# Optimization experiments

Hardware: AMD Instinct MI355X
Metric: run time of the kernel (lower is better)

Reference implementation:

```python
import jax, jax.numpy as jnp
import numpy as np

VOCAB = 8192
BETA = 0.25


def setup_inputs() -> dict:
    key = jax.random.key(0)
    k1, k2 = jax.random.split(key)
    x = jax.random.normal(k1, (16, 1024, 256), dtype=jnp.float32)
    emb = jax.random.normal(k2, (256, VOCAB), dtype=jnp.float32) * 0.05  # xavier-ish scale
    return {"x": x, "emb": emb}


def reference(x, emb):
    C = x.shape[-1]
    x_flat = x.reshape(-1, C)  # [M, C]
    M = x_flat.shape[0]
    distances = ((x_flat ** 2).sum(axis=1, keepdims=True)
                 - 2.0 * jnp.einsum('mc,ck->mk', x_flat, emb)
                 + (emb ** 2).sum(axis=0, keepdims=True))
    # argmax(-d) == argmin(d), same first-occurrence tie-break
    encoding_indices = jnp.argmin(distances, axis=-1)  # [M]
    # direct gather instead of one-hot @ emb (same math)
    quantized = jnp.take(emb, encoding_indices, axis=1).T  # [M, C]
    quantized = quantized.reshape(x.shape)
    e_latent_loss = ((jax.lax.stop_gradient(quantized) - x) ** 2).mean()
    q_latent_loss = ((quantized - jax.lax.stop_gradient(x)) ** 2).mean()
    loss_vq = q_latent_loss + BETA * e_latent_loss
    quantized = x + jax.lax.stop_gradient(quantized - x)  # straight-through
    # avg_probs == one_hot(indices).mean(0) -> normalized histogram
    counts = jnp.zeros((VOCAB,), dtype=x.dtype).at[encoding_indices].add(1.0)
    avg_probs = counts / M
    perplexity = jnp.exp(-jnp.sum(avg_probs * jnp.log(avg_probs + 1e-10)))
    return quantized, loss_vq, perplexity
```

## Files before the change

### kernel.cpp

```cpp
#include <hip/hip_runtime.h>
#include <cfloat>
#include <cmath>

#define VOCAB 8192
#define MTOT 16384
#define CDIM 256
#define BM 64
#define KSPLIT 8
#define KRANGE (VOCAB / KSPLIT)
#define TAU 0.1f
#define IDX_INF 0x7fffffff

typedef __attribute__((ext_vector_type(8))) short bf16x8;
typedef __attribute__((ext_vector_type(4))) float f32x4;

#define AS1 __attribute__((address_space(1)))
#define AS3 __attribute__((address_space(3)))

__device__ __forceinline__ void gl_lds16(const void* g, void* l) {
  __builtin_amdgcn_global_load_lds((const AS1 unsigned int*)g,
                                   (AS3 unsigned int*)l, 16, 0, 0);
}

__device__ inline ushort f2bf(float f) {
  unsigned u = __float_as_uint(f);
  unsigned r = (u + 0x7fffu + ((u >> 16) & 1u)) >> 16;
  return (ushort)r;
}

__device__ __forceinline__ void ins4(uint& k0, uint& k1, uint& k2, uint& k3, uint a) {
  uint t;
  t = min(k0, a); a = max(k0, a); k0 = t;
  t = min(k1, a); a = max(k1, a); k1 = t;
  t = min(k2, a); a = max(k2, a); k2 = t;
  k3 = min(k3, a);
}

__global__ void vq_enorm_kernel(const float* __restrict__ emb,
                                float* __restrict__ enorm16,
                                double* __restrict__ enormd) {
  __shared__ double sd[4][64];
  int tid = threadIdx.x;
  int kk = tid & 63, cg = tid >> 6;
  int k = blockIdx.x * 64 + kk;
  double s = 0.0;
  for (int c = cg * 64; c < cg * 64 + 64; ++c) {
    float v = emb[(size_t)c * VOCAB + k];
    s += (double)v * (double)v;
  }
  sd[cg][kk] = s;
  __syncthreads();
  if (cg == 0) {
    double t = sd[0][kk] + sd[1][kk] + sd[2][kk] + sd[3][kk];
    enorm16[k] = (float)t + 16.0f;
    enormd[k] = t;
  }
}

__global__ void vq_prep_embT_kernel(const float* __restrict__ emb,
                                    float* __restrict__ embT) {
  __shared__ float t[32][33];
  int bc = blockIdx.x & 7;
  int bk = blockIdx.x >> 3;
  int lx = threadIdx.x & 31, lyq = threadIdx.x >> 5;
#pragma unroll
  for (int yy = 0; yy < 4; ++yy) {
    int y = lyq * 4 + yy;
    t[y][lx] = emb[(size_t)(bc * 32 + y) * VOCAB + bk * 32 + lx];
  }
  __syncthreads();
#pragma unroll
  for (int yy = 0; yy < 4; ++yy) {
    int y = lyq * 4 + yy;
    embT[(size_t)(bk * 32 + y) * CDIM + bc * 32 + lx] = t[lx][y];
  }
}

__global__ void vq_pack_x_kernel(const float* __restrict__ x,
                                 ushort* __restrict__ xb) {
  int u = blockIdx.x * 256 + threadIdx.x;
  int rb = u >> 11;
  int q = u & 2047;
  int cc = q >> 9, row = (q >> 3) & 63, sw = q & 7;
  int c0 = cc * 64 + ((sw ^ (row & 7)) << 3);
  const float* src = x + (size_t)(rb * 64 + row) * CDIM + c0;
  float4 v0 = *(const float4*)src;
  float4 v1 = *(const float4*)(src + 4);
  float a[8] = {v0.x, v0.y, v0.z, v0.w, v1.x, v1.y, v1.z, v1.w};
  bf16x8 h;
#pragma unroll
  for (int j = 0; j < 8; ++j) h[j] = (short)f2bf(-2.0f * a[j]);
  *(bf16x8*)(xb + (size_t)u * 8) = h;
}

__global__ void vq_pack_e_kernel(const float* __restrict__ embT,
                                 ushort* __restrict__ eb) {
  int u = blockIdx.x * 256 + threadIdx.x;
  int kbcc = u >> 10;
  int q = u & 1023;
  int code = q >> 3, sw = q & 7;
  int kb2 = kbcc >> 2, cc = kbcc & 3;
  int c0 = cc * 64 + ((sw ^ (code & 7)) << 3);
  const float* src = embT + (size_t)(kb2 * 128 + code) * CDIM + c0;
  float4 v0 = *(const float4*)src;
  float4 v1 = *(const float4*)(src + 4);
  float a[8] = {v0.x, v0.y, v0.z, v0.w, v1.x, v1.y, v1.z, v1.w};
  bf16x8 h;
#pragma unroll
  for (int j = 0; j < 8; ++j) h[j] = (short)f2bf(a[j]);
  *(bf16x8*)(eb + (size_t)u * 8) = h;
}

__global__ __launch_bounds__(256, 2) void vq_dist_bf16_kernel(
    const ushort* __restrict__ xb, const ushort* __restrict__ eb,
    const float* __restrict__ en16g, uint4* __restrict__ pk) {
  __shared__ ushort Asw[4 * 64 * 64];
  __shared__ ushort Bsw[2 * 128 * 64];

  const int tid = threadIdx.x;
  const int lane = tid & 63, wid = tid >> 6;
  const int wr = wid >> 1, wc = wid & 1;
  const int l15 = lane & 15, lg = lane >> 4;
  const int rb = blockIdx.x >> 3, sp = blockIdx.x & 7;
  const int m0 = rb * BM;

  uint baA[2][2], baB[4][2];
#pragma unroll
  for (int mf = 0; mf < 2; ++mf) {
    int row = wr * 32 + mf * 16 + l15;
#pragma unroll
    for (int kh = 0; kh < 2; ++kh)
      baA[mf][kh] = row * 128 + ((((kh * 4) + lg) ^ (row & 7)) << 4);
  }
#pragma unroll
  for (int nf = 0; nf < 4; ++nf) {
    int code = wc * 64 + nf * 16 + l15;
#pragma unroll
    for (int kh = 0; kh < 2; ++kh)
      baB[nf][kh] = code * 128 + ((((kh * 4) + lg) ^ (code & 7)) << 4);
  }

  const uint plB = wid * 2048 + lane * 8;
  const ushort* ebk = eb + (size_t)sp * 262144;

  {
    const ushort* xs = xb + (size_t)rb * 16384;
#pragma unroll
    for (int i = 0; i < 8; ++i) {
      int seg = wid * 8 + i;
      gl_lds16(xs + (size_t)seg * 512 + lane * 8, &Asw[seg * 512]);
    }
#pragma unroll
    for (int i = 0; i < 4; ++i)
      gl_lds16(ebk + plB + i * 512, &Bsw[(wid * 4 + i) * 512]);
  }

  const int nb = sp * KRANGE + wc * 64 + l15;
  uint kmin[8];
#pragma unroll
  for (int s = 0; s < 8; ++s) kmin[s] = 0xffffffffu;

  f32x4 acc[2][4];

  for (int kt = 0; kt < 8; ++kt) {
    float e16[4];
#pragma unroll
    for (int nf = 0; nf < 4; ++nf) e16[nf] = en16g[nb + kt * 128 + nf * 16];
#pragma unroll
    for (int mf = 0; mf < 2; ++mf)
#pragma unroll
      for (int nf = 0; nf < 4; ++nf)
        acc[mf][nf] = (f32x4){e16[nf], e16[nf], e16[nf], e16[nf]};

#pragma unroll
    for (int cc = 0; cc < 4; ++cc) {
      __syncthreads();
      if (cc < 3 || kt < 7) {
        const ushort* src = ebk + (cc + 1) * 8192 + plB;
        ushort* dst = &Bsw[((cc + 1) & 1) * 8192 + (wid * 4) * 512];
#pragma unroll
        for (int i = 0; i < 4; ++i)
          gl_lds16(src + i * 512, dst + i * 512);
      }
      const char* Ab = (const char*)Asw + cc * 8192;
      const char* Bb = (const char*)Bsw + (cc & 1) * 16384;
#pragma unroll
      for (int kh = 0; kh < 2; ++kh) {
        bf16x8 af[2], bfr[4];
#pragma unroll
        for (int mf = 0; mf < 2; ++mf)
          af[mf] = *(const bf16x8*)(Ab + baA[mf][kh]);
#pragma unroll
        for (int nf = 0; nf < 4; ++nf)
          bfr[nf] = *(const bf16x8*)(Bb + baB[nf][kh]);
#pragma unroll
        for (int mf = 0; mf < 2; ++mf)
#pragma unroll
          for (int nf = 0; nf < 4; ++nf)
            acc[mf][nf] = __builtin_amdgcn_mfma_f32_16x16x32_bf16(af[mf], bfr[nf], acc[mf][nf], 0, 0, 0);
      }
    }
#pragma unroll
    for (int nf = 0; nf < 4; ++nf) {
      uint nk = (uint)(nb + kt * 128 + nf * 16);
#pragma unroll
      for (int mf = 0; mf < 2; ++mf)
#pragma unroll
        for (int r = 0; r < 4; ++r) {
          uint u = __float_as_uint(acc[mf][nf][r]) & 0xffffe000u;
          kmin[mf * 4 + r] = min(kmin[mf * 4 + r], u | nk);
        }
    }
    ebk += 32768;
  }

  __syncthreads();
  uint* karr = (uint*)Asw;
#pragma unroll
  for (int mf = 0; mf < 2; ++mf)
#pragma unroll
    for (int r = 0; r < 4; ++r) {
      int row = wr * 32 + mf * 16 + lg * 4 + r;
      karr[(wc * 64 + row) * 17 + l15] = kmin[mf * 4 + r];
    }
  __syncthreads();
  if (tid < BM) {
    uint k0 = ~0u, k1 = ~0u, k2 = ~0u, k3 = ~0u;
    const uint* r0 = karr + tid * 17;
    const uint* r1 = karr + (64 + tid) * 17;
#pragma unroll
    for (int j = 0; j < 16; ++j) ins4(k0, k1, k2, k3, r0[j]);
#pragma unroll
    for (int j = 0; j < 16; ++j) ins4(k0, k1, k2, k3, r1[j]);
    pk[(size_t)sp * MTOT + m0 + tid] = make_uint4(k0, k1, k2, k3);
  }
}

__global__ void vq_gather_kernel(
    const float* __restrict__ x, const float* __restrict__ embT,
    const double* __restrict__ enormd, const uint4* __restrict__ pk,
    float* __restrict__ out, int* __restrict__ counts, float* __restrict__ ssep) {
  const int wid = threadIdx.x >> 6, lane = threadIdx.x & 63;
  const int m = blockIdx.x * 4 + wid;

  const float4 xq = *(const float4*)(x + (size_t)m * CDIM + lane * 4);

  float bd = FLT_MAX, sd = FLT_MAX;
  uint bkey = 0xffffffffu;
#pragma unroll
  for (int sp2 = 0; sp2 < KSPLIT; ++sp2) {
    uint4 kv = pk[(size_t)sp2 * MTOT + m];
    uint ks[4] = {kv.x, kv.y, kv.z, kv.w};
#pragma unroll
    for (int j = 0; j < 4; ++j) {
      uint k = ks[j];
      float dq = __uint_as_float(k & 0xffffe000u);
      if (k < bkey) { sd = bd; bd = dq; bkey = k; }
      else sd = fminf(sd, dq);
    }
  }
  int best = (int)(bkey & 8191u);
  if (sd - bd < TAU) {
    double bD = DBL_MAX;
    int bn = IDX_INF;
    for (int sp2 = 0; sp2 < KSPLIT; ++sp2) {
      uint4 kv = pk[(size_t)sp2 * MTOT + m];
      uint ks[4] = {kv.x, kv.y, kv.z, kv.w};
#pragma unroll
      for (int j = 0; j < 4; ++j) {
        int cj = (int)(ks[j] & 8191u);
        const float4 ev = *(const float4*)(embT + (size_t)cj * CDIM + lane * 4);
        double p = (double)xq.x * ev.x + (double)xq.y * ev.y
                 + (double)xq.z * ev.z + (double)xq.w * ev.w;
#pragma unroll
        for (int off = 1; off < 64; off <<= 1) p += __shfl_xor(p, off, 64);
        double dj = enormd[cj] - 2.0 * p;
        if (dj < bD || (dj == bD && cj < bn)) { bD = dj; bn = cj; }
      }
    }
    best = bn;
  }
  const float4 ev = *(const float4*)(embT + (size_t)best * CDIM + lane * 4);
  *(float4*)(out + (size_t)m * CDIM + lane * 4) = ev;
  float dx = ev.x - xq.x, dy = ev.y - xq.y, dz = ev.z - xq.z, dw = ev.w - xq.w;
  float v = dx * dx + dy * dy + dz * dz + dw * dw;
#pragma unroll
  for (int off = 32; off > 0; off >>= 1) v += __shfl_down(v, off, 64);
  if (lane == 0) {
    ssep[m] = v;
    atomicAdd(&counts[best], 1);
  }
}

__global__ void vq_final1_kernel(const float* __restrict__ ssep,
                                 const int* __restrict__ counts,
                                 double* __restrict__ part) {
  __shared__ double red[256];
  const int tid = threadIdx.x, b = blockIdx.x;
  red[tid] = (double)ssep[b * 256 + tid];
  __syncthreads();
  for (int off = 128; off > 0; off >>= 1) {
    if (tid < off) red[tid] += red[tid + off];
    __syncthreads();
  }
  if (tid == 0) part[b] = red[0];
  __syncthreads();
  double e = 0.0;
  if (tid < 128) {
    double p = (double)counts[b * 128 + tid] / (double)MTOT;
    e = p * log(p + 1e-10);
  }
  red[tid] = e;
  __syncthreads();
  for (int off = 128; off > 0; off >>= 1) {
    if (tid < off) red[tid] += red[tid + off];
    __syncthreads();
  }
  if (tid == 0) part[64 + b] = red[0];
}

__global__ void vq_final2_kernel(const double* __restrict__ part,
                                 float* __restrict__ out) {
  const int lane = threadIdx.x;
  double s = part[lane], e = part[64 + lane];
#pragma unroll
  for (int off = 32; off > 0; off >>= 1) {
    s += __shfl_down(s, off, 64);
    e += __shfl_down(e, off, 64);
  }
  if (lane == 0) {
    out[(size_t)MTOT * CDIM] = (float)(1.25 * s / (double)((size_t)MTOT * CDIM));
    out[(size_t)MTOT * CDIM + 1] = (float)exp(-e);
  }
}

extern "C" void kernel_launch(void* const* d_in, const int* in_sizes, int n_in,
                              void* d_out, int out_size, void* d_ws, size_t ws_size,
                              hipStream_t stream) {
  const float* x = (const float*)d_in[0];
  const float* emb = (const float*)d_in[1];
  float* out = (float*)d_out;
  char* ws = (char*)d_ws;

  double* enormd = (double*)(ws);
  float* enorm16 = (float*)(ws + 65536);
  uint4* pk      = (uint4*)(ws + 98304);
  int* counts    = (int*)(ws + 2195456);
  float* ssep    = (float*)(ws + 2228224);
  double* part   = (double*)(ws + 2293760);
  float* embT    = (float*)(ws + 2294784);
  ushort* xb     = (ushort*)(ws + 10683392);
  ushort* eb     = (ushort*)(ws + 19072000);

  hipMemsetAsync(counts, 0, VOCAB * sizeof(int), stream);
  vq_enorm_kernel<<<VOCAB / 64, 256, 0, stream>>>(emb, enorm16, enormd);
  vq_prep_embT_kernel<<<(VOCAB / 32) * (CDIM / 32), 256, 0, stream>>>(emb, embT);
  vq_pack_e_kernel<<<(VOCAB * CDIM / 8) / 256, 256, 0, stream>>>(embT, eb);
  vq_pack_x_kernel<<<(MTOT * CDIM / 8) / 256, 256, 0, stream>>>(x, xb);
  vq_dist_bf16_kernel<<<(MTOT / BM) * KSPLIT, 256, 0, stream>>>(xb, eb, enorm16, pk);
  vq_gather_kernel<<<MTOT / 4, 256, 0, stream>>>(x, embT, enormd, pk, out, counts, ssep);
  vq_final1_kernel<<<64, 256, 0, stream>>>(ssep, counts, part);
  vq_final2_kernel<<<1, 64, 0, stream>>>(part, out);
}
```

Measured before the change: 169.3 us.

## Enlarge distance GEMM tile to 128 rows with 8 waves and split key storage

Restructures the bf16 distance kernel from 64-row tiles and 4 waves to 128-row tiles with 512 threads, each wave computing a 64x128 sub-tile. The x and embedding packing are reorganised into a new pair-interleaved swizzled layout, so each B chunk is reused across more rows and fewer blocks reload the codebook. The packed float/index keys (masked distance plus +16 offset) are replaced by separate float distance and int index arrays with explicit tie-breaking, and the top-4 candidates are reduced in two stages. This raises register pressure (acc[4][8] plus 16 best slots) and LDS use, and doubles the candidate buffer traffic to the gather kernel.

```diff
diff --git a/kernel.cpp b/kernel.cpp
--- a/kernel.cpp
+++ b/kernel.cpp
@@ -5,9 +5,7 @@
 #define VOCAB 8192
 #define MTOT 16384
 #define CDIM 256
-#define BM 64
 #define KSPLIT 8
-#define KRANGE (VOCAB / KSPLIT)
 #define TAU 0.1f
 #define IDX_INF 0x7fffffff
 
@@ -28,16 +26,8 @@
   return (ushort)r;
 }
 
-__device__ __forceinline__ void ins4(uint& k0, uint& k1, uint& k2, uint& k3, uint a) {
-  uint t;
-  t = min(k0, a); a = max(k0, a); k0 = t;
-  t = min(k1, a); a = max(k1, a); k1 = t;
-  t = min(k2, a); a = max(k2, a); k2 = t;
-  k3 = min(k3, a);
-}
-
 __global__ void vq_enorm_kernel(const float* __restrict__ emb,
-                                float* __restrict__ enorm16,
+                                float* __restrict__ enorm,
                                 double* __restrict__ enormd) {
   __shared__ double sd[4][64];
   int tid = threadIdx.x;
@@ -52,7 +42,7 @@
   __syncthreads();
   if (cg == 0) {
     double t = sd[0][kk] + sd[1][kk] + sd[2][kk] + sd[3][kk];
-    enorm16[k] = (float)t + 16.0f;
+    enorm[k] = (float)t;
     enormd[k] = t;
   }
 }
@@ -79,11 +69,14 @@
 __global__ void vq_pack_x_kernel(const float* __restrict__ x,
                                  ushort* __restrict__ xb) {
   int u = blockIdx.x * 256 + threadIdx.x;
-  int rb = u >> 11;
-  int q = u & 2047;
-  int cc = q >> 9, row = (q >> 3) & 63, sw = q & 7;
-  int c0 = cc * 64 + ((sw ^ (row & 7)) << 3);
-  const float* src = x + (size_t)(rb * 64 + row) * CDIM + c0;
+  int rb = u >> 12;
+  int o = u & 4095;
+  int cc = o >> 9, w = o & 511;
+  int pair = w >> 3, sswz = w & 7;
+  int s = sswz ^ (pair & 7);
+  int row = pair * 2 + (s >> 2);
+  int g = s & 3;
+  const float* src = x + (size_t)(rb * 128 + row) * CDIM + cc * 32 + g * 8;
   float4 v0 = *(const float4*)src;
   float4 v1 = *(const float4*)(src + 4);
   float a[8] = {v0.x, v0.y, v0.z, v0.w, v1.x, v1.y, v1.z, v1.w};
@@ -96,12 +89,18 @@
 __global__ void vq_pack_e_kernel(const float* __restrict__ embT,
                                  ushort* __restrict__ eb) {
   int u = blockIdx.x * 256 + threadIdx.x;
-  int kbcc = u >> 10;
-  int q = u & 1023;
-  int code = q >> 3, sw = q & 7;
-  int kb2 = kbcc >> 2, cc = kbcc & 3;
-  int c0 = cc * 64 + ((sw ^ (code & 7)) << 3);
-  const float* src = embT + (size_t)(kb2 * 128 + code) * CDIM + c0;
+  int sp = u >> 15;
+  int r = u & 32767;
+  int ct = (r >> 14) & 1, chunk = (r >> 11) & 7;
+  int o16 = r & 2047;
+  int wcg = o16 >> 9, w = o16 & 511;
+  int pair = w >> 3, sswz = w & 7;
+  int s = sswz ^ (pair & 7);
+  int cloc = pair * 2 + (s >> 2);
+  int g = s & 3;
+  int code = sp * 1024 + ct * 512 + wcg * 128 + cloc;
+  int dims = chunk * 32 + g * 8;
+  const float* src = embT + (size_t)code * CDIM + dims;
   float4 v0 = *(const float4*)src;
   float4 v1 = *(const float4*)(src + 4);
   float a[8] = {v0.x, v0.y, v0.z, v0.w, v1.x, v1.y, v1.z, v1.w};
@@ -111,134 +110,163 @@
   *(bf16x8*)(eb + (size_t)u * 8) = h;
 }
 
-__global__ __launch_bounds__(256, 2) void vq_dist_bf16_kernel(
+__global__ __launch_bounds__(512, 2) void vq_dist_kernel(
     const ushort* __restrict__ xb, const ushort* __restrict__ eb,
-    const float* __restrict__ en16g, uint4* __restrict__ pk) {
-  __shared__ ushort Asw[4 * 64 * 64];
-  __shared__ ushort Bsw[2 * 128 * 64];
+    const float* __restrict__ enorm,
+    float4* __restrict__ pkd, int4* __restrict__ pki) {
+  __shared__ ushort Abuf[32768];
+  __shared__ ushort Bbuf[2][16384];
 
   const int tid = threadIdx.x;
   const int lane = tid & 63, wid = tid >> 6;
-  const int wr = wid >> 1, wc = wid & 1;
+  const int wr = wid >> 2, wc = wid & 3;
   const int l15 = lane & 15, lg = lane >> 4;
   const int rb = blockIdx.x >> 3, sp = blockIdx.x & 7;
-  const int m0 = rb * BM;
-
-  uint baA[2][2], baB[4][2];
-#pragma unroll
-  for (int mf = 0; mf < 2; ++mf) {
-    int row = wr * 32 + mf * 16 + l15;
-#pragma unroll
-    for (int kh = 0; kh < 2; ++kh)
-      baA[mf][kh] = row * 128 + ((((kh * 4) + lg) ^ (row & 7)) << 4);
-  }
-#pragma unroll
-  for (int nf = 0; nf < 4; ++nf) {
-    int code = wc * 64 + nf * 16 + l15;
-#pragma unroll
-    for (int kh = 0; kh < 2; ++kh)
-      baB[nf][kh] = code * 128 + ((((kh * 4) + lg) ^ (code & 7)) << 4);
-  }
-
-  const uint plB = wid * 2048 + lane * 8;
-  const ushort* ebk = eb + (size_t)sp * 262144;
+  const int m0 = rb * 128;
+  const int spbase = sp * 1024;
 
   {
-    const ushort* xs = xb + (size_t)rb * 16384;
-#pragma unroll
-    for (int i = 0; i < 8; ++i) {
-      int seg = wid * 8 + i;
-      gl_lds16(xs + (size_t)seg * 512 + lane * 8, &Asw[seg * 512]);
-    }
+    const ushort* xs = xb + (size_t)rb * 32768;
+#pragma unroll
+    for (int i = 0; i < 8; ++i)
+      gl_lds16(xs + (wid * 8 + i) * 512 + lane * 8, &Abuf[(wid * 8 + i) * 512]);
+    const ushort* bs = eb + (size_t)sp * 262144;
 #pragma unroll
     for (int i = 0; i < 4; ++i)
-      gl_lds16(ebk + plB + i * 512, &Bsw[(wid * 4 + i) * 512]);
-  }
-
-  const int nb = sp * KRANGE + wc * 64 + l15;
-  uint kmin[8];
-#pragma unroll
-  for (int s = 0; s < 8; ++s) kmin[s] = 0xffffffffu;
-
-  f32x4 acc[2][4];
-
-  for (int kt = 0; kt < 8; ++kt) {
-    float e16[4];
-#pragma unroll
-    for (int nf = 0; nf < 4; ++nf) e16[nf] = en16g[nb + kt * 128 + nf * 16];
-#pragma unroll
-    for (int mf = 0; mf < 2; ++mf)
-#pragma unroll
-      for (int nf = 0; nf < 4; ++nf)
+      gl_lds16(bs + (wid * 4 + i) * 512 + lane * 8, &Bbuf[0][(wid * 4 + i) * 512]);
+  }
+
+  uint offA[4], offB[8];
+#pragma unroll
+  for (int mf = 0; mf < 4; ++mf) {
+    int row = wr * 64 + mf * 16 + l15;
+    int pr = row >> 1, s = ((row & 1) << 2) | lg;
+    offA[mf] = pr * 128 + ((s ^ (pr & 7)) << 4);
+  }
+#pragma unroll
+  for (int nf = 0; nf < 8; ++nf) {
+    int cl = nf * 16 + l15;
+    int pr = cl >> 1, s = ((cl & 1) << 2) | lg;
+    offB[nf] = wc * 8192 + pr * 128 + ((s ^ (pr & 7)) << 4);
+  }
+
+  float bv[16];
+  int bi[16];
+#pragma unroll
+  for (int s = 0; s < 16; ++s) { bv[s] = FLT_MAX; bi[s] = IDX_INF; }
+
+#pragma unroll
+  for (int ct = 0; ct < 2; ++ct) {
+    float e16[8];
+#pragma unroll
+    for (int nf = 0; nf < 8; ++nf)
+      e16[nf] = enorm[spbase + ct * 512 + wc * 128 + nf * 16 + l15];
+    f32x4 acc[4][8];
+#pragma unroll
+    for (int mf = 0; mf < 4; ++mf)
+#pragma unroll
+      for (int nf = 0; nf < 8; ++nf)
         acc[mf][nf] = (f32x4){e16[nf], e16[nf], e16[nf], e16[nf]};
 
 #pragma unroll
-    for (int cc = 0; cc < 4; ++cc) {
+    for (int cc = 0; cc < 8; ++cc) {
+      const int step = ct * 8 + cc;
       __syncthreads();
-      if (cc < 3 || kt < 7) {
-        const ushort* src = ebk + (cc + 1) * 8192 + plB;
-        ushort* dst = &Bsw[((cc + 1) & 1) * 8192 + (wid * 4) * 512];
+      if (step < 15) {
+        const ushort* bs = eb + (size_t)sp * 262144 + (size_t)(step + 1) * 16384;
+        ushort* dst = &Bbuf[(step + 1) & 1][0];
 #pragma unroll
         for (int i = 0; i < 4; ++i)
-          gl_lds16(src + i * 512, dst + i * 512);
+          gl_lds16(bs + (wid * 4 + i) * 512 + lane * 8, dst + (wid * 4 + i) * 512);
       }
-      const char* Ab = (const char*)Asw + cc * 8192;
-      const char* Bb = (const char*)Bsw + (cc & 1) * 16384;
-#pragma unroll
-      for (int kh = 0; kh < 2; ++kh) {
-        bf16x8 af[2], bfr[4];
-#pragma unroll
-        for (int mf = 0; mf < 2; ++mf)
-          af[mf] = *(const bf16x8*)(Ab + baA[mf][kh]);
-#pragma unroll
-        for (int nf = 0; nf < 4; ++nf)
-          bfr[nf] = *(const bf16x8*)(Bb + baB[nf][kh]);
-#pragma unroll
-        for (int mf = 0; mf < 2; ++mf)
-#pragma unroll
-          for (int nf = 0; nf < 4; ++nf)
-            acc[mf][nf] = __builtin_amdgcn_mfma_f32_16x16x32_bf16(af[mf], bfr[nf], acc[mf][nf], 0, 0, 0);
+      const char* Ab = (const char*)Abuf + cc * 8192;
+      const char* Bb = (const char*)&Bbuf[cc & 1][0];
+      bf16x8 af[4];
+#pragma unroll
+      for (int mf = 0; mf < 4; ++mf) af[mf] = *(const bf16x8*)(Ab + offA[mf]);
+#pragma unroll
+      for (int nf = 0; nf < 8; ++nf) {
+        bf16x8 bfr = *(const bf16x8*)(Bb + offB[nf]);
+#pragma unroll
+        for (int mf = 0; mf < 4; ++mf)
+          acc[mf][nf] = __builtin_amdgcn_mfma_f32_16x16x32_bf16(af[mf], bfr, acc[mf][nf], 0, 0, 0);
       }
     }
 #pragma unroll
-    for (int nf = 0; nf < 4; ++nf) {
-      uint nk = (uint)(nb + kt * 128 + nf * 16);
-#pragma unroll
-      for (int mf = 0; mf < 2; ++mf)
+    for (int nf = 0; nf < 8; ++nf) {
+      int n = spbase + ct * 512 + wc * 128 + nf * 16 + l15;
+#pragma unroll
+      for (int mf = 0; mf < 4; ++mf)
 #pragma unroll
         for (int r = 0; r < 4; ++r) {
-          uint u = __float_as_uint(acc[mf][nf][r]) & 0xffffe000u;
-          kmin[mf * 4 + r] = min(kmin[mf * 4 + r], u | nk);
+          float d = acc[mf][nf][r];
+          int s = mf * 4 + r;
+          if (d < bv[s]) { bv[s] = d; bi[s] = n; }
         }
     }
-    ebk += 32768;
-  }
-
-  __syncthreads();
-  uint* karr = (uint*)Asw;
-#pragma unroll
-  for (int mf = 0; mf < 2; ++mf)
+  }
+
+  __syncthreads();
+  float* kd = (float*)Abuf;
+  int* ki = (int*)Abuf + 8192;
+#pragma unroll
+  for (int mf = 0; mf < 4; ++mf)
 #pragma unroll
     for (int r = 0; r < 4; ++r) {
-      int row = wr * 32 + mf * 16 + lg * 4 + r;
-      karr[(wc * 64 + row) * 17 + l15] = kmin[mf * 4 + r];
-    }
-  __syncthreads();
-  if (tid < BM) {
-    uint k0 = ~0u, k1 = ~0u, k2 = ~0u, k3 = ~0u;
-    const uint* r0 = karr + tid * 17;
-    const uint* r1 = karr + (64 + tid) * 17;
-#pragma unroll
-    for (int j = 0; j < 16; ++j) ins4(k0, k1, k2, k3, r0[j]);
-#pragma unroll
-    for (int j = 0; j < 16; ++j) ins4(k0, k1, k2, k3, r1[j]);
-    pk[(size_t)sp * MTOT + m0 + tid] = make_uint4(k0, k1, k2, k3);
+      int row = wr * 64 + mf * 16 + lg * 4 + r;
+      int idx = (wc * 128 + row) * 16 + l15;
+      kd[idx] = bv[mf * 4 + r];
+      ki[idx] = bi[mf * 4 + r];
+    }
+  __syncthreads();
+  float* kod = (float*)&Bbuf[0][0];
+  int* koi = (int*)&Bbuf[0][0] + 1024;
+  {
+    int row = tid >> 2, part = tid & 3;
+    const float* rd = kd + (part * 128 + row) * 16;
+    const int* ri = ki + (part * 128 + row) * 16;
+    float d0 = FLT_MAX, d1 = FLT_MAX;
+    int i0 = IDX_INF, i1 = IDX_INF;
+#pragma unroll
+    for (int j = 0; j < 16; ++j) {
+      float a = rd[j];
+      int ai = ri[j];
+      if (a < d0 || (a == d0 && ai < i0)) { d1 = d0; i1 = i0; d0 = a; i0 = ai; }
+      else if (a < d1 || (a == d1 && ai < i1)) { d1 = a; i1 = ai; }
+    }
+    int o = (row * 4 + part) * 2;
+    kod[o] = d0; kod[o + 1] = d1;
+    koi[o] = i0; koi[o + 1] = i1;
+  }
+  __syncthreads();
+  if (tid < 128) {
+    const float* rd = kod + tid * 8;
+    const int* ri = koi + tid * 8;
+    float d[4] = {FLT_MAX, FLT_MAX, FLT_MAX, FLT_MAX};
+    int ix[4] = {IDX_INF, IDX_INF, IDX_INF, IDX_INF};
+#pragma unroll
+    for (int j = 0; j < 8; ++j) {
+      float a = rd[j];
+      int ai = ri[j];
+#pragma unroll
+      for (int q = 0; q < 4; ++q) {
+        bool lt = (a < d[q]) || (a == d[q] && ai < ix[q]);
+        float td = lt ? d[q] : a;
+        int ti = lt ? ix[q] : ai;
+        d[q] = lt ? a : d[q];
+        ix[q] = lt ? ai : ix[q];
+        a = td; ai = ti;
+      }
+    }
+    pkd[(size_t)sp * MTOT + m0 + tid] = make_float4(d[0], d[1], d[2], d[3]);
+    pki[(size_t)sp * MTOT + m0 + tid] = make_int4(ix[0], ix[1], ix[2], ix[3]);
   }
 }
 
 __global__ void vq_gather_kernel(
     const float* __restrict__ x, const float* __restrict__ embT,
-    const double* __restrict__ enormd, const uint4* __restrict__ pk,
+    const double* __restrict__ enormd,
+    const float4* __restrict__ pkd, const int4* __restrict__ pki,
     float* __restrict__ out, int* __restrict__ counts, float* __restrict__ ssep) {
   const int wid = threadIdx.x >> 6, lane = threadIdx.x & 63;
   const int m = blockIdx.x * 4 + wid;
@@ -246,29 +274,31 @@
   const float4 xq = *(const float4*)(x + (size_t)m * CDIM + lane * 4);
 
   float bd = FLT_MAX, sd = FLT_MAX;
-  uint bkey = 0xffffffffu;
+  int bidx = IDX_INF;
 #pragma unroll
   for (int sp2 = 0; sp2 < KSPLIT; ++sp2) {
-    uint4 kv = pk[(size_t)sp2 * MTOT + m];
-    uint ks[4] = {kv.x, kv.y, kv.z, kv.w};
+    float4 dv = pkd[(size_t)sp2 * MTOT + m];
+    int4 iv = pki[(size_t)sp2 * MTOT + m];
+    float ds[4] = {dv.x, dv.y, dv.z, dv.w};
+    int is[4] = {iv.x, iv.y, iv.z, iv.w};
 #pragma unroll
     for (int j = 0; j < 4; ++j) {
-      uint k = ks[j];
-      float dq = __uint_as_float(k & 0xffffe000u);
-      if (k < bkey) { sd = bd; bd = dq; bkey = k; }
-      else sd = fminf(sd, dq);
-    }
-  }
-  int best = (int)(bkey & 8191u);
+      float dj = ds[j];
+      int ij = is[j];
+      if (dj < bd || (dj == bd && ij < bidx)) { sd = bd; bd = dj; bidx = ij; }
+      else sd = fminf(sd, dj);
+    }
+  }
+  int best = bidx;
   if (sd - bd < TAU) {
     double bD = DBL_MAX;
     int bn = IDX_INF;
     for (int sp2 = 0; sp2 < KSPLIT; ++sp2) {
-      uint4 kv = pk[(size_t)sp2 * MTOT + m];
-      uint ks[4] = {kv.x, kv.y, kv.z, kv.w};
+      int4 iv = pki[(size_t)sp2 * MTOT + m];
+      int is[4] = {iv.x, iv.y, iv.z, iv.w};
 #pragma unroll
       for (int j = 0; j < 4; ++j) {
-        int cj = (int)(ks[j] & 8191u);
+        int cj = is[j];
         const float4 ev = *(const float4*)(embT + (size_t)cj * CDIM + lane * 4);
         double p = (double)xq.x * ev.x + (double)xq.y * ev.y
                  + (double)xq.z * ev.z + (double)xq.w * ev.w;
@@ -343,22 +373,24 @@
   char* ws = (char*)d_ws;
 
   double* enormd = (double*)(ws);
-  float* enorm16 = (float*)(ws + 65536);
-  uint4* pk      = (uint4*)(ws + 98304);
-  int* counts    = (int*)(ws + 2195456);
-  float* ssep    = (float*)(ws + 2228224);
-  double* part   = (double*)(ws + 2293760);
-  float* embT    = (float*)(ws + 2294784);
-  ushort* xb     = (ushort*)(ws + 10683392);
-  ushort* eb     = (ushort*)(ws + 19072000);
+  float* enorm   = (float*)(ws + 65536);
+  float4* pkd    = (float4*)(ws + 98304);
+  int4* pki      = (int4*)(ws + 2195456);
+  int* counts    = (int*)(ws + 4292608);
+  float* ssep    = (float*)(ws + 4325376);
+  double* part   = (double*)(ws + 4390912);
+  float* embT    = (float*)(ws + 4391936);
+  ushort* xb     = (ushort*)(ws + 12780544);
+  ushort* eb     = (ushort*)(ws + 21169152);
 
   hipMemsetAsync(counts, 0, VOCAB * sizeof(int), stream);
-  vq_enorm_kernel<<<VOCAB / 64, 256, 0, stream>>>(emb, enorm16, enormd);
+  vq_enorm_kernel<<<VOCAB / 64, 256, 0, stream>>>(emb, enorm, enormd);
   vq_prep_embT_kernel<<<(VOCAB / 32) * (CDIM / 32), 256, 0, stream>>>(emb, embT);
   vq_pack_e_kernel<<<(VOCAB * CDIM / 8) / 256, 256, 0, stream>>>(embT, eb);
   vq_pack_x_kernel<<<(MTOT * CDIM / 8) / 256, 256, 0, stream>>>(x, xb);
-  vq_dist_bf16_kernel<<<(MTOT / BM) * KSPLIT, 256, 0, stream>>>(xb, eb, enorm16, pk);
-  vq_gather_kernel<<<MTOT / 4, 256, 0, stream>>>(x, embT, enormd, pk, out, counts, ssep);
+  vq_dist_kernel<<<(MTOT / 128) * KSPLIT, 512, 0, stream>>>(xb, eb, enorm, pkd, pki);
+  vq_gather_kernel<<<MTOT / 4, 256, 0, stream>>>(x, embT, enormd, pkd, pki,
+                                                 out, counts, ssep);
   vq_final1_kernel<<<64, 256, 0, stream>>>(ssep, counts, part);
   vq_final2_kernel<<<1, 64, 0, stream>>>(part, out);
 }
```

New measurement: 191.8 us. 1.13x slower.
